# Kernel optimization log

Hardware: AMD Instinct MI355X
Metric: run time of the kernel (lower is better)

Reference implementation:

```python
import jax, jax.numpy as jnp
import numpy as np

B, L, D, NUM_ITEM, NBIN, LAYER_NUM = 1000, 50, 128, 100000, 10, 3


def _gru(x, W_ih, W_hh, b_ih, b_hh):
    # x: [B, L, Din]; torch gate order r,z,n; returns (outputs [B,L,H], h_last [B,H])
    bsz = x.shape[0]
    H = W_hh.shape[1]
    xp = jnp.einsum('bld,gd->blg', x, W_ih) + b_ih  # [B, L, 3H]

    def step(h, xp_t):
        gh = h @ W_hh.T + b_hh
        xr, xz, xn = jnp.split(xp_t, 3, axis=-1)
        hr, hz, hn = jnp.split(gh, 3, axis=-1)
        r = jax.nn.sigmoid(xr + hr)
        z = jax.nn.sigmoid(xz + hz)
        n = jnp.tanh(xn + r * hn)
        h_new = (1.0 - z) * n + z * h
        return h_new, h_new

    h0 = jnp.zeros((bsz, H), x.dtype)
    h_last, outs = jax.lax.scan(step, h0, jnp.swapaxes(xp, 0, 1))
    return jnp.swapaxes(outs, 0, 1), h_last


def _t_gcn(h, edge, edge_weight, layer_num):
    # edge-list weighted propagation; average of all layer outputs (LightGCN-style)
    src, dst = edge[0], edge[1]
    acc = h
    x = h
    for _ in range(layer_num):
        msg = x[src] * edge_weight[:, None]
        x = jax.ops.segment_sum(msg, dst, num_segments=h.shape[0])
        acc = acc + x
    return acc / (layer_num + 1)


def setup_inputs() -> dict:
    rng = np.random.default_rng(0)
    sess_len = (np.arange(B) % L) + 1
    T = int(sess_len.sum())
    seg_ids = np.repeat(np.arange(B), sess_len)
    pos_ids = np.concatenate([np.arange(L - l, L) for l in sess_len])
    n_nodes, n_edges = T, 2 * T

    key = jax.random.key(0)
    ks = jax.random.split(key, 24)
    std = 0.1

    def p(k, shape):
        return (jax.random.normal(k, shape, jnp.float32) * std)

    inp = {
        'items': jnp.asarray(rng.integers(0, NUM_ITEM, n_nodes), jnp.int32),
        'edge': jnp.asarray(rng.integers(0, n_nodes, (2, n_edges)), jnp.int32),
        'edge_weight': jax.random.uniform(ks[0], (n_edges,), jnp.float32),
        'item2idx': jnp.arange(T, dtype=jnp.int32),
        'bins': jnp.asarray(rng.integers(0, NBIN, (B, L)), jnp.int32),
        'seg_ids': jnp.asarray(seg_ids, jnp.int32),
        'pos_ids': jnp.asarray(pos_ids, jnp.int32),
        'sess_len': jnp.asarray(sess_len, jnp.int32),
        'item_emb': p(ks[1], (NUM_ITEM, D)),
        'bin_emb': p(ks[2], (NBIN, D)),
        'Wih_f': p(ks[3], (3 * D, D)), 'Whh_f': p(ks[4], (3 * D, D)),
        'bih_f': p(ks[5], (3 * D,)), 'bhh_f': p(ks[6], (3 * D,)),
        'Wih_b': p(ks[7], (3 * D, D)), 'Whh_b': p(ks[8], (3 * D, D)),
        'bih_b': p(ks[9], (3 * D,)), 'bhh_b': p(ks[10], (3 * D,)),
        'w1': p(ks[11], (1, 2 * D)),
        'w2': p(ks[12], (D, 2 * D)),
        'v3': p(ks[13], (1, D)),
        'Wih_s': p(ks[14], (3 * D, D)), 'Whh_s': p(ks[15], (3 * D, D)),
        'bih_s': p(ks[16], (3 * D,)), 'bhh_s': p(ks[17], (3 * D,)),
        'w3': p(ks[18], (1, D)), 'b3': p(ks[19], (1,)),
    }
    return inp


def reference(items, edge, edge_weight, item2idx, bins, seg_ids, pos_ids, sess_len,
              item_emb, bin_emb,
              Wih_f, Whh_f, bih_f, bhh_f, Wih_b, Whh_b, bih_b, bhh_b,
              w1, w2, v3, Wih_s, Whh_s, bih_s, bhh_s, w3, b3):
    # graph propagation over unique items, gathered back to session tokens
    h = item_emb[items]                                  # [N, D]
    h_final = _t_gcn(h, edge, edge_weight, LAYER_NUM)[item2idx]  # [T, D]

    # time-bin embedding + bidirectional GRU (dropout = identity in eval)
    e = bin_emb[bins]                                    # [B, L, D]
    out_f, _ = _gru(e, Wih_f, Whh_f, bih_f, bhh_f)
    out_b, _ = _gru(e[:, ::-1], Wih_b, Whh_b, bih_b, bhh_b)
    e_dir = jnp.concatenate([out_f, out_b[:, ::-1]], axis=-1)  # [B, L, 2D]

    b_gate = jax.nn.sigmoid(e_dir @ w1.T)                # [B, L, 1]
    e_hat_full = b_gate * e_dir[:, :, :D] + (1.0 - b_gate) * e_dir[:, :, D:]
    # take last sess_len[i] steps of each session -> ragged gather
    e_hat = e_hat_full[seg_ids, pos_ids]                 # [T, D]

    beta = jnp.tanh(jnp.concatenate([h_final, e_hat], axis=-1) @ w2.T) @ v3.T  # [T, 1]
    c = beta * h_final                                   # [T, D]

    z_long = jax.ops.segment_sum(c, seg_ids, num_segments=B)  # [B, D]

    # right-aligned pad then short GRU, keep final hidden
    c_pad = jnp.zeros((B, L, D), c.dtype).at[seg_ids, pos_ids].set(c)
    _, z_short = _gru(c_pad, Wih_s, Whh_s, bih_s, bhh_s)  # [B, D]

    f = jax.nn.sigmoid((z_long + z_short) @ w3.T + b3)   # [B, 1]
    z_final = f * z_long + (1.0 - f) * z_short
    return z_final @ item_emb.T                          # [B, NUM_ITEM]
```

## Files before the change

### kernel.cpp

```cpp
#include <hip/hip_runtime.h>
#include <hip/hip_fp16.h>

#define D    128
#define L    50
#define G3   384
#define NBIN 10

#define FBM 128
#define FBN 128

typedef float f32x4 __attribute__((ext_vector_type(4)));
typedef short s16x8 __attribute__((ext_vector_type(8)));

#define MFMA_B16(a,b,c) __builtin_amdgcn_mfma_f32_16x16x32_bf16(a,b,c,0,0,0)

__device__ __forceinline__ float sigm(float x){ return 1.f/(1.f+__expf(-x)); }
__device__ __forceinline__ float tanh_fast(float x){
  float xx = fminf(fmaxf(x,-15.f),15.f);
  float e  = __expf(2.f*xx);
  return (e-1.f)/(e+1.f);
}

#define SPLIT1(x, hu, lu) { unsigned u_ = __float_as_uint(x); hu = u_ >> 16; \
  float hf_ = __uint_as_float(u_ & 0xffff0000u); float lf_ = (x) - hf_; \
  lu = __float_as_uint(lf_) >> 16; }

__device__ __forceinline__ void split8(f32x4 a, f32x4 b, s16x8& hi, s16x8& lo){
  s16x8 h, l;
#pragma unroll
  for (int i=0;i<4;++i){
    unsigned hu, lu;
    SPLIT1(a[i], hu, lu)
    h[i] = (short)hu; l[i] = (short)lu;
  }
#pragma unroll
  for (int i=0;i<4;++i){
    unsigned hu, lu;
    SPLIT1(b[i], hu, lu)
    h[4+i] = (short)hu; l[4+i] = (short)lu;
  }
  hi = h; lo = l;
}

__global__ void k_prep(const float* __restrict__ bin_emb,
                       const float* __restrict__ Wf, const float* __restrict__ bf,
                       const float* __restrict__ Wb, const float* __restrict__ bb,
                       const float* __restrict__ item_emb, const int* __restrict__ items,
                       float* __restrict__ tabf, float* __restrict__ tabb,
                       float* __restrict__ accA, float* __restrict__ xB,
                       float* __restrict__ cpad, int* __restrict__ tokmap,
                       int* __restrict__ deg,
                       unsigned short* __restrict__ zhi, unsigned short* __restrict__ zlo,
                       long long NG, long long BLD, int BL, int NN){
  const long long r1 = 7680, r2 = r1 + NG, r3 = r2 + BLD, r4 = r3 + BL;
  const long long r5 = r4 + NN;
  const long long ZP = 1024*128;
  const long long total = r5 + 2*ZP;
  for (long long i = (long long)blockIdx.x*256 + threadIdx.x; i < total;
       i += (long long)gridDim.x*256){
    if (i < r1){
      int id = (int)i; int dirr = id / (NBIN*G3); int rr = id % (NBIN*G3);
      int v = rr / G3, g = rr % G3;
      const float* W  = dirr ? Wb : Wf;
      const float* bi = dirr ? bb : bf;
      float a = bi[g];
      for (int d = 0; d < D; ++d) a += bin_emb[v*D+d]*W[g*D+d];
      (dirr ? tabb : tabf)[v*G3+g] = a;
    } else if (i < r2){
      long long k = i - r1;
      int nn = (int)(k>>7), d = (int)(k&127);
      float v = item_emb[(size_t)items[nn]*D + d];
      accA[k] = v; xB[k] = v;
    } else if (i < r3){
      cpad[i - r2] = 0.f;
    } else if (i < r4){
      tokmap[i - r3] = -1;
    } else if (i < r5){
      deg[i - r4] = 0;
    } else {
      long long k = i - r5;
      if (k < ZP) zhi[k] = 0;
      else        zlo[k - ZP] = 0;
    }
  }
}

__global__ void k_count(const int* __restrict__ dst, int* __restrict__ deg, int ne){
  int e = blockIdx.x*256 + threadIdx.x;
  if (e < ne) atomicAdd(&deg[dst[e]], 1);
}
__global__ __launch_bounds__(1024) void k_scan(const int* __restrict__ deg,
                                               int* __restrict__ off, int* __restrict__ cursor,
                                               int nn){
  __shared__ int part[1024];
  int tid = threadIdx.x;
  int chunk = (nn + 1023) >> 10;
  int c0 = tid*chunk;
  int s = 0;
  for (int k = 0; k < chunk; ++k){ int v = c0+k; if (v < nn) s += deg[v]; }
  part[tid] = s; __syncthreads();
  for (int d = 1; d < 1024; d <<= 1){
    int v = (tid >= d) ? part[tid-d] : 0;
    __syncthreads();
    part[tid] += v;
    __syncthreads();
  }
  int run = part[tid] - s;
  for (int k = 0; k < chunk; ++k){
    int v = c0+k;
    if (v < nn){ off[v] = run; cursor[v] = run; run += deg[v]; }
  }
  if (tid == 1023) off[nn] = part[1023];
}
__global__ void k_fill(const int* __restrict__ src, const int* __restrict__ dst,
                       const float* __restrict__ ew, int* __restrict__ cursor,
                       int* __restrict__ csrs, float* __restrict__ csrw, int ne){
  int e = blockIdx.x*256 + threadIdx.x;
  if (e >= ne) return;
  int p = atomicAdd(&cursor[dst[e]], 1);
  csrs[p] = src[e];
  csrw[p] = ew[e];
}
__global__ void k_gath(const float* __restrict__ x, float* __restrict__ xn,
                       float* __restrict__ acc,
                       const int* __restrict__ off, const int* __restrict__ csrs,
                       const float* __restrict__ csrw, int n){
  int i = blockIdx.x*256 + threadIdx.x;
  if (i >= n) return;
  int v = i >> 7, d = i & (D-1);
  int a = off[v], b = off[v+1];
  float s = 0.f;
  for (int k = a; k < b; ++k)
    s += x[(size_t)csrs[k]*D + d] * csrw[k];
  xn[i] = s;
  acc[i] += s;
}

__global__ void k_esplit(const float* __restrict__ emb,
                         unsigned short* __restrict__ ehp, unsigned short* __restrict__ elp,
                         int NI, int nslots){
  for (int s = blockIdx.x*256 + threadIdx.x; s < nslots; s += gridDim.x*256){
    int lane = s & 63;
    int nfw  = (s>>6) & 7;
    int kk   = (s>>9) & 3;
    int ntl  = s >> 11;
    int row  = ntl*128 + (nfw>>2)*64 + (nfw&3)*16 + (lane&15);
    int d0   = kk*32 + (lane>>4)*8;
    s16x8 h8 = {0,0,0,0,0,0,0,0}, l8 = h8;
    if (row < NI){
      const f32x4* src = (const f32x4*)&emb[(size_t)row*D + d0];
      split8(src[0], src[1], h8, l8);
    }
    *(s16x8*)&ehp[(size_t)s*8] = h8;
    *(s16x8*)&elp[(size_t)s*8] = l8;
  }
}

__global__ __launch_bounds__(512) void k_gru_fb(
    const float* __restrict__ Whh_f, const float* __restrict__ Whh_b,
    const float* __restrict__ bhh_f, const float* __restrict__ bhh_b,
    const float* __restrict__ tabf,  const float* __restrict__ tabb,
    const int*   __restrict__ bins,  int Bn,
    float* __restrict__ outf, float* __restrict__ outbrev){
  const int dir = blockIdx.y;
  const int b0  = blockIdx.x * 16;
  const float* Whh = dir ? Whh_b : Whh_f;
  const float* bhh = dir ? bhh_b : bhh_f;
  const float* tab = dir ? tabb  : tabf;
  float* outp = dir ? outbrev : outf;

  __shared__ unsigned short hhi[16*128];
  __shared__ unsigned short hlo[16*128];
  __shared__ float xts[NBIN*G3];
  __shared__ int   binr[16][L];

  const int tid = threadIdx.x;
  const int wv = tid>>6, lane = tid&63;
  const int l15 = lane&15, lk = lane>>4;
  const int jb = wv*16;
  const int jq = jb + lk*4;

  s16x8 whi[3][4], wlo[3][4];
#pragma unroll
  for (int g3i = 0; g3i < 3; ++g3i)
#pragma unroll
    for (int ks = 0; ks < 4; ++ks){
      const f32x4* s = (const f32x4*)&Whh[(size_t)(g3i*D + jb + l15)*D + ks*32 + lk*8];
      split8(s[0], s[1], whi[g3i][ks], wlo[g3i][ks]);
    }
  f32x4 bhv[3];
#pragma unroll
  for (int g3i = 0; g3i < 3; ++g3i) bhv[g3i] = *(const f32x4*)&bhh[g3i*D + jq];

  for (int i = tid; i < NBIN*G3; i += 512) xts[i] = tab[i];
  for (int i = tid; i < 16*L; i += 512){
    int r = i / L, t = i % L;
    binr[r][t] = (b0 + r < Bn) ? bins[(b0+r)*L + (dir ? (L-1-t) : t)] : 0;
  }
  for (int i = tid; i < 16*128; i += 512){ hhi[i] = 0; hlo[i] = 0; }

  const int sess = l15;
  const bool sv = (b0 + sess) < Bn;
  float hreg[4] = {0.f,0.f,0.f,0.f};
  const int wbyte = sess*256 + (((jq>>3) ^ (sess&7))<<4) + ((jq&7)<<1);
  __syncthreads();

  for (int t = 0; t < L; ++t){
    f32x4 c0 = {0.f,0.f,0.f,0.f}, c1 = c0, c2 = c0;
#pragma unroll
    for (int ks = 0; ks < 4; ++ks){
      int off = l15*256 + ((((ks<<2)+lk) ^ (l15&7)) << 4);
      s16x8 bh8 = *(const s16x8*)((const char*)hhi + off);
      s16x8 bl8 = *(const s16x8*)((const char*)hlo + off);
      c0 = MFMA_B16(whi[0][ks], bh8, c0); c0 = MFMA_B16(whi[0][ks], bl8, c0); c0 = MFMA_B16(wlo[0][ks], bh8, c0);
      c1 = MFMA_B16(whi[1][ks], bh8, c1); c1 = MFMA_B16(whi[1][ks], bl8, c1); c1 = MFMA_B16(wlo[1][ks], bh8, c1);
      c2 = MFMA_B16(whi[2][ks], bh8, c2); c2 = MFMA_B16(whi[2][ks], bl8, c2); c2 = MFMA_B16(wlo[2][ks], bh8, c2);
    }
    __syncthreads();
    int bin = binr[sess][t];
    const float* xb = &xts[bin*G3];
    f32x4 xr4 = *(const f32x4*)&xb[jq];
    f32x4 xz4 = *(const f32x4*)&xb[D + jq];
    f32x4 xn4 = *(const f32x4*)&xb[2*D + jq];
    ushort4 hi4, lo4;
    f32x4 hn4;
#pragma unroll
    for (int qq = 0; qq < 4; ++qq){
      float gr = c0[qq] + bhv[0][qq];
      float gz = c1[qq] + bhv[1][qq];
      float gn = c2[qq] + bhv[2][qq];
      float rr = sigm(xr4[qq] + gr);
      float zz = sigm(xz4[qq] + gz);
      float nn = tanh_fast(xn4[qq] + rr*gn);
      float hnew = (1.f-zz)*nn + zz*hreg[qq];
      hreg[qq] = hnew;
      unsigned hu, lu; SPLIT1(hnew, hu, lu)
      ((unsigned short*)&hi4)[qq] = (unsigned short)hu;
      ((unsigned short*)&lo4)[qq] = (unsigned short)lu;
      hn4[qq] = hnew;
    }
    *(ushort4*)((char*)hhi + wbyte) = hi4;
    *(ushort4*)((char*)hlo + wbyte) = lo4;
    if (sv){
      float4 o = make_float4(hn4[0],hn4[1],hn4[2],hn4[3]);
      *(float4*)&outp[((size_t)(b0+sess)*L + (dir ? (L-1-t) : t))*D + jq] = o;
    }
    __syncthreads();
  }
}

__global__ __launch_bounds__(512) void k_beta2(
    const float* __restrict__ outf, const float* __restrict__ outbrev,
    const float* __restrict__ accA, const int* __restrict__ idxmap,
    const float* __restrict__ w1, const float* __restrict__ w2,
    const float* __restrict__ v3,
    const int* __restrict__ seg, const int* __restrict__ pos, int T,
    float* __restrict__ c_pad, int* __restrict__ tokmap){
  __shared__ unsigned short Bhi[32*256];
  __shared__ unsigned short Blo[32*256];
  __shared__ float w1s[2*D];
  __shared__ float betas[32];

  const int tid = threadIdx.x;
  const int wv = tid>>6, lane = tid&63;
  const int l15 = lane&15, lk = lane>>4;

  s16x8 w2hi[8], w2lo[8];
#pragma unroll
  for (int ks = 0; ks < 8; ++ks){
    const f32x4* s = (const f32x4*)&w2[(size_t)(wv*16 + l15)*256 + ks*32 + lk*8];
    split8(s[0], s[1], w2hi[ks], w2lo[ks]);
  }
  f32x4 v3q = *(const f32x4*)&v3[wv*16 + lk*4];
  for (int i = tid; i < 2*D; i += 512) w1s[i] = w1[i];
  __syncthreads();

  const int tok = tid >> 4;
  const int d0  = (tid & 15) * 8;
  const int sw  = (tid & 15) ^ (tok & 7);
  const int ntiles = (T + 31) >> 5;

  for (int tile = blockIdx.x; tile < ntiles; tile += gridDim.x){
    int t = tile*32 + tok;
    bool valid = (t < T);
    int sp = 0;
    f32x4 ef0 = {0,0,0,0}, ef1 = ef0, eb0 = ef0, eb1 = ef0, hf0 = ef0, hf1 = ef0;
    if (valid){
      sp = seg[t]*L + pos[t];
      const f32x4* pf = (const f32x4*)&outf[(size_t)sp*D + d0];
      const f32x4* pb = (const f32x4*)&outbrev[(size_t)sp*D + d0];
      const f32x4* ph = (const f32x4*)&accA[(size_t)idxmap[t]*D + d0];
      ef0 = pf[0]; ef1 = pf[1];
      eb0 = pb[0]; eb1 = pb[1];
      hf0 = ph[0]; hf1 = ph[1];
#pragma unroll
      for (int k=0;k<4;++k){ hf0[k]*=0.25f; hf1[k]*=0.25f; }
    }
    float p = 0.f;
#pragma unroll
    for (int k=0;k<4;++k){
      p += ef0[k]*w1s[d0+k]     + eb0[k]*w1s[D+d0+k];
      p += ef1[k]*w1s[d0+4+k]   + eb1[k]*w1s[D+d0+4+k];
    }
    p += __shfl_xor(p,1); p += __shfl_xor(p,2);
    p += __shfl_xor(p,4); p += __shfl_xor(p,8);
    float gate = sigm(p);
    f32x4 eh0, eh1;
#pragma unroll
    for (int k=0;k<4;++k){
      eh0[k] = gate*ef0[k] + (1.f-gate)*eb0[k];
      eh1[k] = gate*ef1[k] + (1.f-gate)*eb1[k];
    }
    {
      s16x8 h8, l8;
      split8(hf0, hf1, h8, l8);
      int byte = tok*512 + (sw<<4);
      *(s16x8*)((char*)Bhi + byte) = h8;
      *(s16x8*)((char*)Blo + byte) = l8;
      split8(eh0, eh1, h8, l8);
      byte = tok*512 + ((16+((tid&15)^(tok&7)))<<4);
      *(s16x8*)((char*)Bhi + byte) = h8;
      *(s16x8*)((char*)Blo + byte) = l8;
    }
    if (tid < 32) betas[tid] = 0.f;
    __syncthreads();
#pragma unroll
    for (int tt = 0; tt < 2; ++tt){
      f32x4 c = {0.f,0.f,0.f,0.f};
#pragma unroll
      for (int ks = 0; ks < 8; ++ks){
        int s_ = ((ks<<2)+lk);
        int off = (tt*16 + l15)*512 + ((s_ ^ (l15&7)) << 4);
        s16x8 bh8 = *(const s16x8*)((const char*)Bhi + off);
        s16x8 bl8 = *(const s16x8*)((const char*)Blo + off);
        c = MFMA_B16(w2hi[ks], bh8, c);
        c = MFMA_B16(w2hi[ks], bl8, c);
        c = MFMA_B16(w2lo[ks], bh8, c);
      }
      float pv = 0.f;
#pragma unroll
      for (int qq = 0; qq < 4; ++qq) pv += tanh_fast(c[qq]) * v3q[qq];
      pv += __shfl_xor(pv, 16);
      pv += __shfl_xor(pv, 32);
      if (lk == 0) atomicAdd(&betas[tt*16 + l15], pv);
    }
    __syncthreads();
    if (valid){
      float beta = betas[tok];
      f32x4 c0, c1;
#pragma unroll
      for (int k=0;k<4;++k){ c0[k] = beta*hf0[k]; c1[k] = beta*hf1[k]; }
      f32x4* pc = (f32x4*)&c_pad[(size_t)sp*D + d0];
      pc[0] = c0; pc[1] = c1;
      if ((tid & 15) == 0) tokmap[sp] = t;
    }
    __syncthreads();
  }
}

__global__ void k_zlong(const float* __restrict__ c_pad, float* __restrict__ zl, int Bn){
  int i = blockIdx.x*256 + threadIdx.x;
  if (i >= Bn*D) return;
  int b = i >> 7, j = i & (D-1);
  float s = 0.f;
  for (int l = 0; l < L; ++l) s += c_pad[((size_t)b*L + l)*D + j];
  zl[i] = s;
}

__global__ __launch_bounds__(512) void k_xps2(
    const float* __restrict__ c_pad, const int* __restrict__ seg,
    const int* __restrict__ pos, const float* __restrict__ Wih,
    const float* __restrict__ bih, int T, float* __restrict__ xps){
  __shared__ unsigned short Bhi[32*128];
  __shared__ unsigned short Blo[32*128];
  __shared__ float us[32*388];
  __shared__ float bihs[G3];

  const int tid = threadIdx.x;
  const int wv = tid>>6, lane = tid&63;
  const int l15 = lane&15, lk = lane>>4;
  const int gbase = wv * 48;

  s16x8 whi[3][4], wlo[3][4];
#pragma unroll
  for (int mt = 0; mt < 3; ++mt)
#pragma unroll
    for (int ks = 0; ks < 4; ++ks){
      const f32x4* s = (const f32x4*)&Wih[(size_t)(gbase + mt*16 + l15)*D + ks*32 + lk*8];
      split8(s[0], s[1], whi[mt][ks], wlo[mt][ks]);
    }
  for (int i = tid; i < G3; i += 512) bihs[i] = bih[i];
  __syncthreads();

  const int tok = tid >> 4;
  const int d0  = (tid & 15) * 8;
  const int ntiles = (T + 31) >> 5;

  for (int tile = blockIdx.x; tile < ntiles; tile += gridDim.x){
    int t = tile*32 + tok;
    bool valid = (t < T);
    f32x4 x0 = {0,0,0,0}, x1 = x0;
    if (valid){
      int sp = seg[t]*L + pos[t];
      const f32x4* pc = (const f32x4*)&c_pad[(size_t)sp*D + d0];
      x0 = pc[0]; x1 = pc[1];
    }
    {
      s16x8 h8, l8;
      split8(x0, x1, h8, l8);
      int byte = tok*256 + ((((tid&15)) ^ (tok&7))<<4);
      *(s16x8*)((char*)Bhi + byte) = h8;
      *(s16x8*)((char*)Blo + byte) = l8;
    }
    __syncthreads();
#pragma unroll
    for (int tt = 0; tt < 2; ++tt){
      f32x4 c[3];
#pragma unroll
      for (int mt = 0; mt < 3; ++mt){ f32x4 z = {0,0,0,0}; c[mt] = z; }
#pragma unroll
      for (int ks = 0; ks < 4; ++ks){
        int off = (tt*16 + l15)*256 + ((((ks<<2)+lk) ^ (l15&7)) << 4);
        s16x8 bh8 = *(const s16x8*)((const char*)Bhi + off);
        s16x8 bl8 = *(const s16x8*)((const char*)Blo + off);
        c[0] = MFMA_B16(whi[0][ks], bh8, c[0]); c[0] = MFMA_B16(whi[0][ks], bl8, c[0]); c[0] = MFMA_B16(wlo[0][ks], bh8, c[0]);
        c[1] = MFMA_B16(whi[1][ks], bh8, c[1]); c[1] = MFMA_B16(whi[1][ks], bl8, c[1]); c[1] = MFMA_B16(wlo[1][ks], bh8, c[1]);
        c[2] = MFMA_B16(whi[2][ks], bh8, c[2]); c[2] = MFMA_B16(whi[2][ks], bl8, c[2]); c[2] = MFMA_B16(wlo[2][ks], bh8, c[2]);
      }
#pragma unroll
      for (int mt = 0; mt < 3; ++mt)
        *(f32x4*)&us[(tt*16 + l15)*388 + gbase + mt*16 + lk*4] = c[mt];
    }
    __syncthreads();
    for (int i4 = tid; i4 < 32*96; i4 += 512){
      int tk = i4 / 96, g4 = (i4 % 96) * 4;
      int tt2 = tile*32 + tk;
      if (tt2 < T){
        f32x4 u4 = *(const f32x4*)&us[tk*388 + g4];
        f32x4 b4 = *(const f32x4*)&bihs[g4];
#pragma unroll
        for (int k=0;k<4;++k) u4[k] += b4[k];
        *(f32x4*)&xps[(size_t)tt2*G3 + g4] = u4;
      }
    }
    __syncthreads();
  }
}

__global__ __launch_bounds__(512) void k_grus(
    const float* __restrict__ Whh, const float* __restrict__ bhh,
    const float* __restrict__ bih,
    const float* __restrict__ xps, const int* __restrict__ tokmap,
    const float* __restrict__ zl, const float* __restrict__ w3,
    const float* __restrict__ b3, int Bn,
    unsigned short* __restrict__ zhi, unsigned short* __restrict__ zlo){
  const int b0 = blockIdx.x * 16;

  __shared__ unsigned short hhi[16*128];
  __shared__ unsigned short hlo[16*128];
  __shared__ int   maprow[16][L];
  __shared__ float redg[16];

  const int tid = threadIdx.x;
  const int wv = tid>>6, lane = tid&63;
  const int l15 = lane&15, lk = lane>>4;
  const int jb = wv*16;
  const int jq = jb + lk*4;

  s16x8 whi[3][4], wlo[3][4];
#pragma unroll
  for (int g3i = 0; g3i < 3; ++g3i)
#pragma unroll
    for (int ks = 0; ks < 4; ++ks){
      const f32x4* s = (const f32x4*)&Whh[(size_t)(g3i*D + jb + l15)*D + ks*32 + lk*8];
      split8(s[0], s[1], whi[g3i][ks], wlo[g3i][ks]);
    }
  f32x4 bhv[3], biv[3];
#pragma unroll
  for (int g3i = 0; g3i < 3; ++g3i){
    bhv[g3i] = *(const f32x4*)&bhh[g3i*D + jq];
    biv[g3i] = *(const f32x4*)&bih[g3i*D + jq];
  }
  for (int i = tid; i < 16*L; i += 512){
    int r = i / L, t = i % L;
    maprow[r][t] = (b0 + r < Bn) ? tokmap[(b0+r)*L + t] : -1;
  }
  for (int i = tid; i < 16*128; i += 512){ hhi[i] = 0; hlo[i] = 0; }

  const int sess = l15;
  const bool sv = (b0 + sess) < Bn;
  float hreg[4] = {0.f,0.f,0.f,0.f};
  const int wbyte = sess*256 + (((jq>>3) ^ (sess&7))<<4) + ((jq&7)<<1);
  __syncthreads();

  for (int t = 0; t < L; ++t){
    int tok = maprow[sess][t];
    f32x4 xr4, xz4, xn4;
    if (tok >= 0){
      const float* xb = &xps[(size_t)tok*G3];
      xr4 = *(const f32x4*)&xb[jq];
      xz4 = *(const f32x4*)&xb[D + jq];
      xn4 = *(const f32x4*)&xb[2*D + jq];
    } else { xr4 = biv[0]; xz4 = biv[1]; xn4 = biv[2]; }
    f32x4 c0 = {0.f,0.f,0.f,0.f}, c1 = c0, c2 = c0;
#pragma unroll
    for (int ks = 0; ks < 4; ++ks){
      int off = l15*256 + ((((ks<<2)+lk) ^ (l15&7)) << 4);
      s16x8 bh8 = *(const s16x8*)((const char*)hhi + off);
      s16x8 bl8 = *(const s16x8*)((const char*)hlo + off);
      c0 = MFMA_B16(whi[0][ks], bh8, c0); c0 = MFMA_B16(whi[0][ks], bl8, c0); c0 = MFMA_B16(wlo[0][ks], bh8, c0);
      c1 = MFMA_B16(whi[1][ks], bh8, c1); c1 = MFMA_B16(whi[1][ks], bl8, c1); c1 = MFMA_B16(wlo[1][ks], bh8, c1);
      c2 = MFMA_B16(whi[2][ks], bh8, c2); c2 = MFMA_B16(whi[2][ks], bl8, c2); c2 = MFMA_B16(wlo[2][ks], bh8, c2);
    }
    __syncthreads();
    ushort4 hi4, lo4;
#pragma unroll
    for (int qq = 0; qq < 4; ++qq){
      float gr = c0[qq] + bhv[0][qq];
      float gz = c1[qq] + bhv[1][qq];
      float gn = c2[qq] + bhv[2][qq];
      float rr = sigm(xr4[qq] + gr);
      float zz = sigm(xz4[qq] + gz);
      float nn = tanh_fast(xn4[qq] + rr*gn);
      float hnew = (1.f-zz)*nn + zz*hreg[qq];
      hreg[qq] = hnew;
      unsigned hu, lu; SPLIT1(hnew, hu, lu)
      ((unsigned short*)&hi4)[qq] = (unsigned short)hu;
      ((unsigned short*)&lo4)[qq] = (unsigned short)lu;
    }
    *(ushort4*)((char*)hhi + wbyte) = hi4;
    *(ushort4*)((char*)hlo + wbyte) = lo4;
    __syncthreads();
  }

  if (tid < 16) redg[tid] = 0.f;
  __syncthreads();
  f32x4 zl4 = {0.f,0.f,0.f,0.f};
  if (sv) zl4 = *(const f32x4*)&zl[(size_t)(b0+sess)*D + jq];
  f32x4 w34 = *(const f32x4*)&w3[jq];
  float part = 0.f;
#pragma unroll
  for (int qq = 0; qq < 4; ++qq) part += (zl4[qq] + hreg[qq]) * w34[qq];
  if (sv) atomicAdd(&redg[sess], part);
  __syncthreads();
  if (sv){
    float f = sigm(redg[sess] + b3[0]);
    ushort4 h4, l4;
#pragma unroll
    for (int qq = 0; qq < 4; ++qq){
      float zv = f*zl4[qq] + (1.f-f)*hreg[qq];
      unsigned hu, lu; SPLIT1(zv, hu, lu)
      ((unsigned short*)&h4)[qq] = (unsigned short)hu;
      ((unsigned short*)&l4)[qq] = (unsigned short)lu;
    }
    int row = b0 + sess;
    int mtile = row >> 7, r128 = row & 127;
    int wmr = r128 >> 6, mfr = (r128 >> 4) & 3, l15r = r128 & 15;
    int kkr = jq >> 5, lkr = (jq & 31) >> 3, e0 = jq & 7;
    int laner = lkr*16 + l15r;
    size_t slot = ((size_t)(((mtile*4 + kkr)*2 + wmr)*4 + mfr))*64 + laner;
    *(ushort4*)&zhi[slot*8 + e0] = h4;
    *(ushort4*)&zlo[slot*8 + e0] = l4;
  }
}

__global__ __launch_bounds__(256, 3) void k_fmm(
    const unsigned short* __restrict__ zhi, const unsigned short* __restrict__ zlo,
    const unsigned short* __restrict__ ehp, const unsigned short* __restrict__ elp,
    float* __restrict__ out, int NI, int Bsz){
  __shared__ float fs[64*136];

  int nwg = gridDim.x;
  int hw  = blockIdx.x;
  int q8 = nwg >> 3, r8 = nwg & 7;
  int xcd = hw & 7, idx = hw >> 3;
  int logical = (xcd < r8 ? xcd*(q8+1) : r8*(q8+1) + (xcd-r8)*q8) + idx;
  int ntile = logical >> 3;
  int mtile = logical & 7;
  int m0 = mtile*FBM;
  int n0 = ntile*FBN;

  const int t    = threadIdx.x;
  const int lane = t & 63;
  const int wid  = t >> 6;
  const int wm   = wid >> 1, wn = wid & 1;
  const int l15  = lane & 15, lk = lane >> 4;

  f32x4 acc[4][4];
#pragma unroll
  for (int i = 0; i < 4; ++i)
#pragma unroll
    for (int jj = 0; jj < 4; ++jj){ f32x4 z4 = {0.f,0.f,0.f,0.f}; acc[i][jj] = z4; }

#pragma unroll
  for (int kk = 0; kk < 4; ++kk){
    s16x8 ah[4], al[4], bh8[4], bl8[4];
#pragma unroll
    for (int mf = 0; mf < 4; ++mf){
      size_t slot = ((size_t)(((mtile*4 + kk)*2 + wm)*4 + mf))*64 + lane;
      ah[mf] = *(const s16x8*)&zhi[slot*8];
      al[mf] = *(const s16x8*)&zlo[slot*8];
    }
#pragma unroll
    for (int nf = 0; nf < 4; ++nf){
      size_t slot = ((size_t)((ntile*4 + kk)*8 + wn*4 + nf))*64 + lane;
      bh8[nf] = *(const s16x8*)&ehp[slot*8];
      bl8[nf] = *(const s16x8*)&elp[slot*8];
    }
#pragma unroll
    for (int mf = 0; mf < 4; ++mf)
#pragma unroll
      for (int nf = 0; nf < 4; ++nf){
        acc[mf][nf] = MFMA_B16(ah[mf], bh8[nf], acc[mf][nf]);
        acc[mf][nf] = MFMA_B16(ah[mf], bl8[nf], acc[mf][nf]);
        acc[mf][nf] = MFMA_B16(al[mf], bh8[nf], acc[mf][nf]);
      }
  }

#pragma unroll
  for (int p = 0; p < 2; ++p){
    __syncthreads();
    if (wm == p){
#pragma unroll
      for (int mf = 0; mf < 4; ++mf)
#pragma unroll
        for (int nf = 0; nf < 4; ++nf)
#pragma unroll
          for (int qq = 0; qq < 4; ++qq)
            fs[(mf*16 + lk*4 + qq)*136 + wn*64 + nf*16 + l15] = acc[mf][nf][qq];
    }
    __syncthreads();
#pragma unroll
    for (int it = 0; it < 8; ++it){
      int row = (t>>5) + it*8;
      int col = (t&31)*4;
      f32x4 v = *(const f32x4*)&fs[row*136 + col];
      int gr = m0 + p*64 + row;
      if (gr < Bsz && n0 + col < NI)
        __builtin_nontemporal_store(v, (f32x4*)&out[(size_t)gr*NI + n0 + col]);
    }
  }
}

extern "C" void kernel_launch(void* const* d_in, const int* in_sizes, int n_in,
                              void* d_out, int out_size, void* d_ws, size_t ws_size,
                              hipStream_t stream){
  const int*   items    = (const int*)d_in[0];
  const int*   edge     = (const int*)d_in[1];
  const float* ew       = (const float*)d_in[2];
  const int*   item2idx = (const int*)d_in[3];
  const int*   bins     = (const int*)d_in[4];
  const int*   seg      = (const int*)d_in[5];
  const int*   pos      = (const int*)d_in[6];
  const float* item_emb = (const float*)d_in[8];
  const float* bin_emb  = (const float*)d_in[9];
  const float* Wih_f = (const float*)d_in[10];
  const float* Whh_f = (const float*)d_in[11];
  const float* bih_f = (const float*)d_in[12];
  const float* bhh_f = (const float*)d_in[13];
  const float* Wih_b = (const float*)d_in[14];
  const float* Whh_b = (const float*)d_in[15];
  const float* bih_b = (const float*)d_in[16];
  const float* bhh_b = (const float*)d_in[17];
  const float* w1    = (const float*)d_in[18];
  const float* w2    = (const float*)d_in[19];
  const float* v3    = (const float*)d_in[20];
  const float* Wih_s = (const float*)d_in[21];
  const float* Whh_s = (const float*)d_in[22];
  const float* bih_s = (const float*)d_in[23];
  const float* bhh_s = (const float*)d_in[24];
  const float* w3    = (const float*)d_in[25];
  const float* b3    = (const float*)d_in[26];
  float* out = (float*)d_out;

  const int NN = in_sizes[0];
  const int NE = in_sizes[2];
  const int T  = in_sizes[3];
  const int B  = in_sizes[7];
  const int NI = in_sizes[8] / D;

  const size_t NG  = (size_t)NN * D;
  const size_t BLD = (size_t)B * L * D;
  const int ntilesN = (NI + FBN - 1)/FBN;
  const int nslots  = ntilesN * 2048;

  float* ws   = (float*)d_ws;
  float* accA = ws;
  float* xB   = ws + NG;
  float* xC   = ws + 2*NG;
  float* xps  = ws;
  float* outf = ws + 3*NG;
  float* outb = outf + BLD;
  unsigned short* ehp = (unsigned short*)outf;
  unsigned short* elp = ehp + (size_t)nslots*8;
  float* cpad = outb + BLD;
  int*   tokmap = (int*)(cpad + BLD);
  float* tabf = (float*)(tokmap + (size_t)B*L);
  float* tabb = tabf + NBIN*G3;
  float* zl   = tabb + NBIN*G3;
  unsigned short* zhi = (unsigned short*)(zl + (size_t)B*D);
  unsigned short* zlo = zhi + 1024*128;
  int* deg    = (int*)(zlo + 1024*128);
  int* off    = deg + NN;
  int* cursor = off + NN + 1;
  int* csrs   = cursor + NN;
  float* csrw = (float*)(csrs + NE);

  hipLaunchKernelGGL(k_prep, dim3(2048), dim3(256), 0, stream,
                     bin_emb, Wih_f, bih_f, Wih_b, bih_b, item_emb, items,
                     tabf, tabb, accA, xB, cpad, tokmap, deg, zhi, zlo,
                     (long long)NG, (long long)BLD, B*L, NN);
  hipLaunchKernelGGL(k_count, dim3((NE+255)/256), dim3(256), 0, stream, edge+NE, deg, NE);
  hipLaunchKernelGGL(k_scan, dim3(1), dim3(1024), 0, stream, deg, off, cursor, NN);
  hipLaunchKernelGGL(k_fill, dim3((NE+255)/256), dim3(256), 0, stream,
                     edge, edge+NE, ew, cursor, csrs, csrw, NE);
  const int ggrid = (int)((NG + 255)/256);
  hipLaunchKernelGGL(k_gath, dim3(ggrid), dim3(256), 0, stream, xB, xC, accA, off, csrs, csrw, (int)NG);
  hipLaunchKernelGGL(k_gath, dim3(ggrid), dim3(256), 0, stream, xC, xB, accA, off, csrs, csrw, (int)NG);
  hipLaunchKernelGGL(k_gath, dim3(ggrid), dim3(256), 0, stream, xB, xC, accA, off, csrs, csrw, (int)NG);
  hipLaunchKernelGGL(k_gru_fb, dim3((B+15)/16, 2), dim3(512), 0, stream,
                     Whh_f, Whh_b, bhh_f, bhh_b, tabf, tabb, bins, B, outf, outb);
  hipLaunchKernelGGL(k_beta2, dim3(256), dim3(512), 0, stream,
                     outf, outb, accA, item2idx, w1, w2, v3, seg, pos, T, cpad, tokmap);
  hipLaunchKernelGGL(k_zlong, dim3((B*D+255)/256), dim3(256), 0, stream, cpad, zl, B);
  hipLaunchKernelGGL(k_xps2, dim3(256), dim3(512), 0, stream,
                     cpad, seg, pos, Wih_s, bih_s, T, xps);
  hipLaunchKernelGGL(k_esplit, dim3(2048), dim3(256), 0, stream,
                     item_emb, ehp, elp, NI, nslots);
  hipLaunchKernelGGL(k_grus, dim3((B+15)/16), dim3(512), 0, stream,
                     Whh_s, bhh_s, bih_s, xps, tokmap, zl, w3, b3, B, zhi, zlo);
  {
    int mtiles = (B + FBM - 1)/FBM;
    hipLaunchKernelGGL(k_fmm, dim3(mtiles*ntilesN), dim3(256), 0, stream,
                       zhi, zlo, ehp, elp, out, NI, B);
  }
}
```

Measured before the change: 480.2 us.

## Double-buffer GRU hidden state, fuse CSR build, overlap embedding split with short GRU

The GRU kernels now ping-pong the hidden-state LDS buffers, which removes one barrier per timestep, and each matvec is split into two independent accumulator chains for more MFMA ILP. Degree counting moves into shared-memory atomics inside a single-block CSR kernel, and the separate zero-fill of deg is dropped. z_long is folded into k_xps2, and the item-embedding hi/lo split runs on spare blocks of the short-GRU launch so it overlaps the latency-bound recurrence. Together these cut launch count and serialization. The trade-offs are a single-block edge count of about 50k atomics, and ehp/elp moving to a fresh workspace region.

```diff
diff --git a/kernel.cpp b/kernel.cpp
--- a/kernel.cpp
+++ b/kernel.cpp
@@ -5,6 +5,7 @@
 #define L    50
 #define G3   384
 #define NBIN 10
+#define NNMAX 25600
 
 #define FBM 128
 #define FBN 128
@@ -49,13 +50,11 @@
                        float* __restrict__ tabf, float* __restrict__ tabb,
                        float* __restrict__ accA, float* __restrict__ xB,
                        float* __restrict__ cpad, int* __restrict__ tokmap,
-                       int* __restrict__ deg,
                        unsigned short* __restrict__ zhi, unsigned short* __restrict__ zlo,
-                       long long NG, long long BLD, int BL, int NN){
+                       long long NG, long long BLD, int BL){
   const long long r1 = 7680, r2 = r1 + NG, r3 = r2 + BLD, r4 = r3 + BL;
-  const long long r5 = r4 + NN;
   const long long ZP = 1024*128;
-  const long long total = r5 + 2*ZP;
+  const long long total = r4 + 2*ZP;
   for (long long i = (long long)blockIdx.x*256 + threadIdx.x; i < total;
        i += (long long)gridDim.x*256){
     if (i < r1){
@@ -75,29 +74,28 @@
       cpad[i - r2] = 0.f;
     } else if (i < r4){
       tokmap[i - r3] = -1;
-    } else if (i < r5){
-      deg[i - r4] = 0;
     } else {
-      long long k = i - r5;
+      long long k = i - r4;
       if (k < ZP) zhi[k] = 0;
       else        zlo[k - ZP] = 0;
     }
   }
 }
 
-__global__ void k_count(const int* __restrict__ dst, int* __restrict__ deg, int ne){
-  int e = blockIdx.x*256 + threadIdx.x;
-  if (e < ne) atomicAdd(&deg[dst[e]], 1);
-}
-__global__ __launch_bounds__(1024) void k_scan(const int* __restrict__ deg,
+__global__ __launch_bounds__(1024) void k_csr1(const int* __restrict__ dst,
                                                int* __restrict__ off, int* __restrict__ cursor,
-                                               int nn){
+                                               int nn, int ne){
+  __shared__ int degs[NNMAX];
   __shared__ int part[1024];
   int tid = threadIdx.x;
+  for (int i = tid; i < nn; i += 1024) degs[i] = 0;
+  __syncthreads();
+  for (int e = tid; e < ne; e += 1024) atomicAdd(&degs[dst[e]], 1);
+  __syncthreads();
   int chunk = (nn + 1023) >> 10;
   int c0 = tid*chunk;
   int s = 0;
-  for (int k = 0; k < chunk; ++k){ int v = c0+k; if (v < nn) s += deg[v]; }
+  for (int k = 0; k < chunk; ++k){ int v = c0+k; if (v < nn) s += degs[v]; }
   part[tid] = s; __syncthreads();
   for (int d = 1; d < 1024; d <<= 1){
     int v = (tid >= d) ? part[tid-d] : 0;
@@ -108,7 +106,7 @@
   int run = part[tid] - s;
   for (int k = 0; k < chunk; ++k){
     int v = c0+k;
-    if (v < nn){ off[v] = run; cursor[v] = run; run += deg[v]; }
+    if (v < nn){ off[v] = run; cursor[v] = run; run += degs[v]; }
   }
   if (tid == 1023) off[nn] = part[1023];
 }
@@ -136,26 +134,6 @@
   acc[i] += s;
 }
 
-__global__ void k_esplit(const float* __restrict__ emb,
-                         unsigned short* __restrict__ ehp, unsigned short* __restrict__ elp,
-                         int NI, int nslots){
-  for (int s = blockIdx.x*256 + threadIdx.x; s < nslots; s += gridDim.x*256){
-    int lane = s & 63;
-    int nfw  = (s>>6) & 7;
-    int kk   = (s>>9) & 3;
-    int ntl  = s >> 11;
-    int row  = ntl*128 + (nfw>>2)*64 + (nfw&3)*16 + (lane&15);
-    int d0   = kk*32 + (lane>>4)*8;
-    s16x8 h8 = {0,0,0,0,0,0,0,0}, l8 = h8;
-    if (row < NI){
-      const f32x4* src = (const f32x4*)&emb[(size_t)row*D + d0];
-      split8(src[0], src[1], h8, l8);
-    }
-    *(s16x8*)&ehp[(size_t)s*8] = h8;
-    *(s16x8*)&elp[(size_t)s*8] = l8;
-  }
-}
-
 __global__ __launch_bounds__(512) void k_gru_fb(
     const float* __restrict__ Whh_f, const float* __restrict__ Whh_b,
     const float* __restrict__ bhh_f, const float* __restrict__ bhh_b,
@@ -169,8 +147,8 @@
   const float* tab = dir ? tabb  : tabf;
   float* outp = dir ? outbrev : outf;
 
-  __shared__ unsigned short hhi[16*128];
-  __shared__ unsigned short hlo[16*128];
+  __shared__ unsigned short hhi[2*16*128];
+  __shared__ unsigned short hlo[2*16*128];
   __shared__ float xts[NBIN*G3];
   __shared__ int   binr[16][L];
 
@@ -197,26 +175,37 @@
     int r = i / L, t = i % L;
     binr[r][t] = (b0 + r < Bn) ? bins[(b0+r)*L + (dir ? (L-1-t) : t)] : 0;
   }
-  for (int i = tid; i < 16*128; i += 512){ hhi[i] = 0; hlo[i] = 0; }
+  for (int i = tid; i < 2*16*128; i += 512){ hhi[i] = 0; hlo[i] = 0; }
 
   const int sess = l15;
   const bool sv = (b0 + sess) < Bn;
   float hreg[4] = {0.f,0.f,0.f,0.f};
   const int wbyte = sess*256 + (((jq>>3) ^ (sess&7))<<4) + ((jq&7)<<1);
+  int cur = 0;
   __syncthreads();
 
   for (int t = 0; t < L; ++t){
-    f32x4 c0 = {0.f,0.f,0.f,0.f}, c1 = c0, c2 = c0;
-#pragma unroll
-    for (int ks = 0; ks < 4; ++ks){
-      int off = l15*256 + ((((ks<<2)+lk) ^ (l15&7)) << 4);
+    f32x4 c0a={0.f,0.f,0.f,0.f}, c1a=c0a, c2a=c0a, c0b=c0a, c1b=c0a, c2b=c0a;
+    const int rb = cur*4096;
+#pragma unroll
+    for (int ks = 0; ks < 2; ++ks){
+      int off = rb + l15*256 + ((((ks<<2)+lk) ^ (l15&7)) << 4);
       s16x8 bh8 = *(const s16x8*)((const char*)hhi + off);
       s16x8 bl8 = *(const s16x8*)((const char*)hlo + off);
-      c0 = MFMA_B16(whi[0][ks], bh8, c0); c0 = MFMA_B16(whi[0][ks], bl8, c0); c0 = MFMA_B16(wlo[0][ks], bh8, c0);
-      c1 = MFMA_B16(whi[1][ks], bh8, c1); c1 = MFMA_B16(whi[1][ks], bl8, c1); c1 = MFMA_B16(wlo[1][ks], bh8, c1);
-      c2 = MFMA_B16(whi[2][ks], bh8, c2); c2 = MFMA_B16(whi[2][ks], bl8, c2); c2 = MFMA_B16(wlo[2][ks], bh8, c2);
-    }
-    __syncthreads();
+      c0a = MFMA_B16(whi[0][ks], bh8, c0a); c0a = MFMA_B16(whi[0][ks], bl8, c0a); c0a = MFMA_B16(wlo[0][ks], bh8, c0a);
+      c1a = MFMA_B16(whi[1][ks], bh8, c1a); c1a = MFMA_B16(whi[1][ks], bl8, c1a); c1a = MFMA_B16(wlo[1][ks], bh8, c1a);
+      c2a = MFMA_B16(whi[2][ks], bh8, c2a); c2a = MFMA_B16(whi[2][ks], bl8, c2a); c2a = MFMA_B16(wlo[2][ks], bh8, c2a);
+    }
+#pragma unroll
+    for (int ks = 2; ks < 4; ++ks){
+      int off = rb + l15*256 + ((((ks<<2)+lk) ^ (l15&7)) << 4);
+      s16x8 bh8 = *(const s16x8*)((const char*)hhi + off);
+      s16x8 bl8 = *(const s16x8*)((const char*)hlo + off);
+      c0b = MFMA_B16(whi[0][ks], bh8, c0b); c0b = MFMA_B16(whi[0][ks], bl8, c0b); c0b = MFMA_B16(wlo[0][ks], bh8, c0b);
+      c1b = MFMA_B16(whi[1][ks], bh8, c1b); c1b = MFMA_B16(whi[1][ks], bl8, c1b); c1b = MFMA_B16(wlo[1][ks], bh8, c1b);
+      c2b = MFMA_B16(whi[2][ks], bh8, c2b); c2b = MFMA_B16(whi[2][ks], bl8, c2b); c2b = MFMA_B16(wlo[2][ks], bh8, c2b);
+    }
+    f32x4 c0 = c0a + c0b, c1 = c1a + c1b, c2 = c2a + c2b;
     int bin = binr[sess][t];
     const float* xb = &xts[bin*G3];
     f32x4 xr4 = *(const f32x4*)&xb[jq];
@@ -239,13 +228,15 @@
       ((unsigned short*)&lo4)[qq] = (unsigned short)lu;
       hn4[qq] = hnew;
     }
-    *(ushort4*)((char*)hhi + wbyte) = hi4;
-    *(ushort4*)((char*)hlo + wbyte) = lo4;
+    int wb = (cur^1)*4096 + wbyte;
+    *(ushort4*)((char*)hhi + wb) = hi4;
+    *(ushort4*)((char*)hlo + wb) = lo4;
     if (sv){
       float4 o = make_float4(hn4[0],hn4[1],hn4[2],hn4[3]);
       *(float4*)&outp[((size_t)(b0+sess)*L + (dir ? (L-1-t) : t))*D + jq] = o;
     }
     __syncthreads();
+    cur ^= 1;
   }
 }
 
@@ -326,17 +317,28 @@
     __syncthreads();
 #pragma unroll
     for (int tt = 0; tt < 2; ++tt){
-      f32x4 c = {0.f,0.f,0.f,0.f};
-#pragma unroll
-      for (int ks = 0; ks < 8; ++ks){
+      f32x4 ca = {0.f,0.f,0.f,0.f}, cb = ca;
+#pragma unroll
+      for (int ks = 0; ks < 4; ++ks){
         int s_ = ((ks<<2)+lk);
         int off = (tt*16 + l15)*512 + ((s_ ^ (l15&7)) << 4);
         s16x8 bh8 = *(const s16x8*)((const char*)Bhi + off);
         s16x8 bl8 = *(const s16x8*)((const char*)Blo + off);
-        c = MFMA_B16(w2hi[ks], bh8, c);
-        c = MFMA_B16(w2hi[ks], bl8, c);
-        c = MFMA_B16(w2lo[ks], bh8, c);
+        ca = MFMA_B16(w2hi[ks], bh8, ca);
+        ca = MFMA_B16(w2hi[ks], bl8, ca);
+        ca = MFMA_B16(w2lo[ks], bh8, ca);
       }
+#pragma unroll
+      for (int ks = 4; ks < 8; ++ks){
+        int s_ = ((ks<<2)+lk);
+        int off = (tt*16 + l15)*512 + ((s_ ^ (l15&7)) << 4);
+        s16x8 bh8 = *(const s16x8*)((const char*)Bhi + off);
+        s16x8 bl8 = *(const s16x8*)((const char*)Blo + off);
+        cb = MFMA_B16(w2hi[ks], bh8, cb);
+        cb = MFMA_B16(w2hi[ks], bl8, cb);
+        cb = MFMA_B16(w2lo[ks], bh8, cb);
+      }
+      f32x4 c = ca + cb;
       float pv = 0.f;
 #pragma unroll
       for (int qq = 0; qq < 4; ++qq) pv += tanh_fast(c[qq]) * v3q[qq];
@@ -358,19 +360,11 @@
   }
 }
 
-__global__ void k_zlong(const float* __restrict__ c_pad, float* __restrict__ zl, int Bn){
-  int i = blockIdx.x*256 + threadIdx.x;
-  if (i >= Bn*D) return;
-  int b = i >> 7, j = i & (D-1);
-  float s = 0.f;
-  for (int l = 0; l < L; ++l) s += c_pad[((size_t)b*L + l)*D + j];
-  zl[i] = s;
-}
-
 __global__ __launch_bounds__(512) void k_xps2(
     const float* __restrict__ c_pad, const int* __restrict__ seg,
     const int* __restrict__ pos, const float* __restrict__ Wih,
-    const float* __restrict__ bih, int T, float* __restrict__ xps){
+    const float* __restrict__ bih, int T, float* __restrict__ xps,
+    float* __restrict__ zl, int Bn){
   __shared__ unsigned short Bhi[32*128];
   __shared__ unsigned short Blo[32*128];
   __shared__ float us[32*388];
@@ -380,6 +374,13 @@
   const int wv = tid>>6, lane = tid&63;
   const int l15 = lane&15, lk = lane>>4;
   const int gbase = wv * 48;
+
+  for (int i = blockIdx.x*512 + tid; i < Bn*D; i += gridDim.x*512){
+    int b = i >> 7, j = i & (D-1);
+    float s = 0.f;
+    for (int l = 0; l < L; ++l) s += c_pad[((size_t)b*L + l)*D + j];
+    zl[i] = s;
+  }
 
   s16x8 whi[3][4], wlo[3][4];
 #pragma unroll
@@ -415,21 +416,32 @@
     __syncthreads();
 #pragma unroll
     for (int tt = 0; tt < 2; ++tt){
-      f32x4 c[3];
-#pragma unroll
-      for (int mt = 0; mt < 3; ++mt){ f32x4 z = {0,0,0,0}; c[mt] = z; }
-#pragma unroll
-      for (int ks = 0; ks < 4; ++ks){
+      f32x4 ca[3], cb[3];
+#pragma unroll
+      for (int mt = 0; mt < 3; ++mt){ f32x4 z = {0,0,0,0}; ca[mt] = z; cb[mt] = z; }
+#pragma unroll
+      for (int ks = 0; ks < 2; ++ks){
         int off = (tt*16 + l15)*256 + ((((ks<<2)+lk) ^ (l15&7)) << 4);
         s16x8 bh8 = *(const s16x8*)((const char*)Bhi + off);
         s16x8 bl8 = *(const s16x8*)((const char*)Blo + off);
-        c[0] = MFMA_B16(whi[0][ks], bh8, c[0]); c[0] = MFMA_B16(whi[0][ks], bl8, c[0]); c[0] = MFMA_B16(wlo[0][ks], bh8, c[0]);
-        c[1] = MFMA_B16(whi[1][ks], bh8, c[1]); c[1] = MFMA_B16(whi[1][ks], bl8, c[1]); c[1] = MFMA_B16(wlo[1][ks], bh8, c[1]);
-        c[2] = MFMA_B16(whi[2][ks], bh8, c[2]); c[2] = MFMA_B16(whi[2][ks], bl8, c[2]); c[2] = MFMA_B16(wlo[2][ks], bh8, c[2]);
+        ca[0] = MFMA_B16(whi[0][ks], bh8, ca[0]); ca[0] = MFMA_B16(whi[0][ks], bl8, ca[0]); ca[0] = MFMA_B16(wlo[0][ks], bh8, ca[0]);
+        ca[1] = MFMA_B16(whi[1][ks], bh8, ca[1]); ca[1] = MFMA_B16(whi[1][ks], bl8, ca[1]); ca[1] = MFMA_B16(wlo[1][ks], bh8, ca[1]);
+        ca[2] = MFMA_B16(whi[2][ks], bh8, ca[2]); ca[2] = MFMA_B16(whi[2][ks], bl8, ca[2]); ca[2] = MFMA_B16(wlo[2][ks], bh8, ca[2]);
       }
 #pragma unroll
-      for (int mt = 0; mt < 3; ++mt)
-        *(f32x4*)&us[(tt*16 + l15)*388 + gbase + mt*16 + lk*4] = c[mt];
+      for (int ks = 2; ks < 4; ++ks){
+        int off = (tt*16 + l15)*256 + ((((ks<<2)+lk) ^ (l15&7)) << 4);
+        s16x8 bh8 = *(const s16x8*)((const char*)Bhi + off);
+        s16x8 bl8 = *(const s16x8*)((const char*)Blo + off);
+        cb[0] = MFMA_B16(whi[0][ks], bh8, cb[0]); cb[0] = MFMA_B16(whi[0][ks], bl8, cb[0]); cb[0] = MFMA_B16(wlo[0][ks], bh8, cb[0]);
+        cb[1] = MFMA_B16(whi[1][ks], bh8, cb[1]); cb[1] = MFMA_B16(whi[1][ks], bl8, cb[1]); cb[1] = MFMA_B16(wlo[1][ks], bh8, cb[1]);
+        cb[2] = MFMA_B16(whi[2][ks], bh8, cb[2]); cb[2] = MFMA_B16(whi[2][ks], bl8, cb[2]); cb[2] = MFMA_B16(wlo[2][ks], bh8, cb[2]);
+      }
+#pragma unroll
+      for (int mt = 0; mt < 3; ++mt){
+        f32x4 c = ca[mt] + cb[mt];
+        *(f32x4*)&us[(tt*16 + l15)*388 + gbase + mt*16 + lk*4] = c;
+      }
     }
     __syncthreads();
     for (int i4 = tid; i4 < 32*96; i4 += 512){
@@ -453,11 +465,33 @@
     const float* __restrict__ xps, const int* __restrict__ tokmap,
     const float* __restrict__ zl, const float* __restrict__ w3,
     const float* __restrict__ b3, int Bn,
-    unsigned short* __restrict__ zhi, unsigned short* __restrict__ zlo){
+    unsigned short* __restrict__ zhi, unsigned short* __restrict__ zlo,
+    const float* __restrict__ emb,
+    unsigned short* __restrict__ ehp, unsigned short* __restrict__ elp,
+    int NI, int nslots, int nGru){
+  if (blockIdx.x >= nGru){
+    int nb = gridDim.x - nGru;
+    for (int s = (blockIdx.x - nGru)*512 + threadIdx.x; s < nslots; s += nb*512){
+      int lane = s & 63;
+      int nfw  = (s>>6) & 7;
+      int kk   = (s>>9) & 3;
+      int ntl  = s >> 11;
+      int row  = ntl*128 + (nfw>>2)*64 + (nfw&3)*16 + (lane&15);
+      int d0   = kk*32 + (lane>>4)*8;
+      s16x8 h8 = {0,0,0,0,0,0,0,0}, l8 = h8;
+      if (row < NI){
+        const f32x4* src = (const f32x4*)&emb[(size_t)row*D + d0];
+        split8(src[0], src[1], h8, l8);
+      }
+      *(s16x8*)&ehp[(size_t)s*8] = h8;
+      *(s16x8*)&elp[(size_t)s*8] = l8;
+    }
+    return;
+  }
   const int b0 = blockIdx.x * 16;
 
-  __shared__ unsigned short hhi[16*128];
-  __shared__ unsigned short hlo[16*128];
+  __shared__ unsigned short hhi[2*16*128];
+  __shared__ unsigned short hlo[2*16*128];
   __shared__ int   maprow[16][L];
   __shared__ float redg[16];
 
@@ -485,12 +519,13 @@
     int r = i / L, t = i % L;
     maprow[r][t] = (b0 + r < Bn) ? tokmap[(b0+r)*L + t] : -1;
   }
-  for (int i = tid; i < 16*128; i += 512){ hhi[i] = 0; hlo[i] = 0; }
+  for (int i = tid; i < 2*16*128; i += 512){ hhi[i] = 0; hlo[i] = 0; }
 
   const int sess = l15;
   const bool sv = (b0 + sess) < Bn;
   float hreg[4] = {0.f,0.f,0.f,0.f};
   const int wbyte = sess*256 + (((jq>>3) ^ (sess&7))<<4) + ((jq&7)<<1);
+  int cur = 0;
   __syncthreads();
 
   for (int t = 0; t < L; ++t){
@@ -502,17 +537,27 @@
       xz4 = *(const f32x4*)&xb[D + jq];
       xn4 = *(const f32x4*)&xb[2*D + jq];
     } else { xr4 = biv[0]; xz4 = biv[1]; xn4 = biv[2]; }
-    f32x4 c0 = {0.f,0.f,0.f,0.f}, c1 = c0, c2 = c0;
-#pragma unroll
-    for (int ks = 0; ks < 4; ++ks){
-      int off = l15*256 + ((((ks<<2)+lk) ^ (l15&7)) << 4);
+    f32x4 c0a={0.f,0.f,0.f,0.f}, c1a=c0a, c2a=c0a, c0b=c0a, c1b=c0a, c2b=c0a;
+    const int rb = cur*4096;
+#pragma unroll
+    for (int ks = 0; ks < 2; ++ks){
+      int off = rb + l15*256 + ((((ks<<2)+lk) ^ (l15&7)) << 4);
       s16x8 bh8 = *(const s16x8*)((const char*)hhi + off);
       s16x8 bl8 = *(const s16x8*)((const char*)hlo + off);
-      c0 = MFMA_B16(whi[0][ks], bh8, c0); c0 = MFMA_B16(whi[0][ks], bl8, c0); c0 = MFMA_B16(wlo[0][ks], bh8, c0);
-      c1 = MFMA_B16(whi[1][ks], bh8, c1); c1 = MFMA_B16(whi[1][ks], bl8, c1); c1 = MFMA_B16(wlo[1][ks], bh8, c1);
-      c2 = MFMA_B16(whi[2][ks], bh8, c2); c2 = MFMA_B16(whi[2][ks], bl8, c2); c2 = MFMA_B16(wlo[2][ks], bh8, c2);
-    }
-    __syncthreads();
+      c0a = MFMA_B16(whi[0][ks], bh8, c0a); c0a = MFMA_B16(whi[0][ks], bl8, c0a); c0a = MFMA_B16(wlo[0][ks], bh8, c0a);
+      c1a = MFMA_B16(whi[1][ks], bh8, c1a); c1a = MFMA_B16(whi[1][ks], bl8, c1a); c1a = MFMA_B16(wlo[1][ks], bh8, c1a);
+      c2a = MFMA_B16(whi[2][ks], bh8, c2a); c2a = MFMA_B16(whi[2][ks], bl8, c2a); c2a = MFMA_B16(wlo[2][ks], bh8, c2a);
+    }
+#pragma unroll
+    for (int ks = 2; ks < 4; ++ks){
+      int off = rb + l15*256 + ((((ks<<2)+lk) ^ (l15&7)) << 4);
+      s16x8 bh8 = *(const s16x8*)((const char*)hhi + off);
+      s16x8 bl8 = *(const s16x8*)((const char*)hlo + off);
+      c0b = MFMA_B16(whi[0][ks], bh8, c0b); c0b = MFMA_B16(whi[0][ks], bl8, c0b); c0b = MFMA_B16(wlo[0][ks], bh8, c0b);
+      c1b = MFMA_B16(whi[1][ks], bh8, c1b); c1b = MFMA_B16(whi[1][ks], bl8, c1b); c1b = MFMA_B16(wlo[1][ks], bh8, c1b);
+      c2b = MFMA_B16(whi[2][ks], bh8, c2b); c2b = MFMA_B16(whi[2][ks], bl8, c2b); c2b = MFMA_B16(wlo[2][ks], bh8, c2b);
+    }
+    f32x4 c0 = c0a + c0b, c1 = c1a + c1b, c2 = c2a + c2b;
     ushort4 hi4, lo4;
 #pragma unroll
     for (int qq = 0; qq < 4; ++qq){
@@ -528,9 +573,11 @@
       ((unsigned short*)&hi4)[qq] = (unsigned short)hu;
       ((unsigned short*)&lo4)[qq] = (unsigned short)lu;
     }
-    *(ushort4*)((char*)hhi + wbyte) = hi4;
-    *(ushort4*)((char*)hlo + wbyte) = lo4;
-    __syncthreads();
+    int wb = (cur^1)*4096 + wbyte;
+    *(ushort4*)((char*)hhi + wb) = hi4;
+    *(ushort4*)((char*)hlo + wb) = lo4;
+    __syncthreads();
+    cur ^= 1;
   }
 
   if (tid < 16) redg[tid] = 0.f;
@@ -691,8 +738,6 @@
   float* xps  = ws;
   float* outf = ws + 3*NG;
   float* outb = outf + BLD;
-  unsigned short* ehp = (unsigned short*)outf;
-  unsigned short* elp = ehp + (size_t)nslots*8;
   float* cpad = outb + BLD;
   int*   tokmap = (int*)(cpad + BLD);
   float* tabf = (float*)(tokmap + (size_t)B*L);
@@ -700,18 +745,18 @@
   float* zl   = tabb + NBIN*G3;
   unsigned short* zhi = (unsigned short*)(zl + (size_t)B*D);
   unsigned short* zlo = zhi + 1024*128;
-  int* deg    = (int*)(zlo + 1024*128);
-  int* off    = deg + NN;
+  int* off    = (int*)(zlo + 1024*128);
   int* cursor = off + NN + 1;
   int* csrs   = cursor + NN;
   float* csrw = (float*)(csrs + NE);
+  unsigned short* ehp = (unsigned short*)(csrw + NE);
+  unsigned short* elp = ehp + (size_t)nslots*8;
 
   hipLaunchKernelGGL(k_prep, dim3(2048), dim3(256), 0, stream,
                      bin_emb, Wih_f, bih_f, Wih_b, bih_b, item_emb, items,
-                     tabf, tabb, accA, xB, cpad, tokmap, deg, zhi, zlo,
-                     (long long)NG, (long long)BLD, B*L, NN);
-  hipLaunchKernelGGL(k_count, dim3((NE+255)/256), dim3(256), 0, stream, edge+NE, deg, NE);
-  hipLaunchKernelGGL(k_scan, dim3(1), dim3(1024), 0, stream, deg, off, cursor, NN);
+                     tabf, tabb, accA, xB, cpad, tokmap, zhi, zlo,
+                     (long long)NG, (long long)BLD, B*L);
+  hipLaunchKernelGGL(k_csr1, dim3(1), dim3(1024), 0, stream, edge+NE, off, cursor, NN, NE);
   hipLaunchKernelGGL(k_fill, dim3((NE+255)/256), dim3(256), 0, stream,
                      edge, edge+NE, ew, cursor, csrs, csrw, NE);
   const int ggrid = (int)((NG + 255)/256);
@@ -722,13 +767,14 @@
                      Whh_f, Whh_b, bhh_f, bhh_b, tabf, tabb, bins, B, outf, outb);
   hipLaunchKernelGGL(k_beta2, dim3(256), dim3(512), 0, stream,
                      outf, outb, accA, item2idx, w1, w2, v3, seg, pos, T, cpad, tokmap);
-  hipLaunchKernelGGL(k_zlong, dim3((B*D+255)/256), dim3(256), 0, stream, cpad, zl, B);
   hipLaunchKernelGGL(k_xps2, dim3(256), dim3(512), 0, stream,
-                     cpad, seg, pos, Wih_s, bih_s, T, xps);
-  hipLaunchKernelGGL(k_esplit, dim3(2048), dim3(256), 0, stream,
-                     item_emb, ehp, elp, NI, nslots);
-  hipLaunchKernelGGL(k_grus, dim3((B+15)/16), dim3(512), 0, stream,
-                     Whh_s, bhh_s, bih_s, xps, tokmap, zl, w3, b3, B, zhi, zlo);
+                     cpad, seg, pos, Wih_s, bih_s, T, xps, zl, B);
+  {
+    int nGru = (B + 15)/16;
+    hipLaunchKernelGGL(k_grus, dim3(256), dim3(512), 0, stream,
+                       Whh_s, bhh_s, bih_s, xps, tokmap, zl, w3, b3, B, zhi, zlo,
+                       item_emb, ehp, elp, NI, nslots, nGru);
+  }
   {
     int mtiles = (B + FBM - 1)/FBM;
     hipLaunchKernelGGL(k_fmm, dim3(mtiles*ntilesN), dim3(256), 0, stream,
```

Result: faster. 446.3 us, median of 2 (-7.1%).
